# Kernel tuning notes

Measured on AMD Instinct MI355X. Metric: run time of the kernel, lower is better.

The kernel has to match this reference:

```python
import jax, jax.numpy as jnp
import numpy as np
from jax import lax

# norse LIFParameters defaults: dt=1e-3, tau_mem_inv=100, tau_syn_inv=200, v_leak=0, v_reset=0
ALPHA = 100.0
DT_TM = 0.1   # dt * tau_mem_inv
DT_TS = 0.2   # dt * tau_syn_inv

@jax.custom_vjp
def superspike(x):
    # Heaviside forward, SuperSpike surrogate gradient backward
    return (x > 0).astype(x.dtype)

def _ss_fwd(x):
    return superspike(x), x

def _ss_bwd(x, g):
    return (g / (ALPHA * jnp.abs(x) + 1.0) ** 2,)

superspike.defvjp(_ss_fwd, _ss_bwd)

def lif_step(inp, v, i, v_th):
    # norse lif_feed_forward_step (feedforward LIF cell)
    v_dec = v + DT_TM * (i - v)           # v_leak = 0
    i_dec = i * (1.0 - DT_TS)
    z = superspike(v_dec - v_th)
    v_new = (1.0 - z) * v_dec             # reset to v_reset = 0 on spike
    return z, v_new, i_dec + inp

def conv2d(x, w):
    return lax.conv_general_dilated(x, w, (1, 1), 'VALID',
                                    dimension_numbers=('NCHW', 'OIHW', 'NCHW'))

def avg_pool2(x):
    s = lax.reduce_window(x, jnp.zeros((), x.dtype), lax.add,
                          (1, 1, 2, 2), (1, 1, 2, 2), 'VALID')
    return s * jnp.asarray(0.25, x.dtype)

def setup_inputs() -> dict:
    key = jax.random.key(0)
    ks = jax.random.split(key, 6)
    x = jax.random.uniform(ks[0], (40, 256, 1, 28, 28), dtype=jnp.float32)
    # kaiming-ish scales (1/sqrt(fan_in))
    w_conv1 = jax.random.normal(ks[1], (20, 1, 3, 3), jnp.float32) * (1.0 / np.sqrt(9))
    w_conv2 = jax.random.normal(ks[2], (50, 20, 3, 3), jnp.float32) * (1.0 / np.sqrt(180))
    w_fc1 = jax.random.normal(ks[3], (500, 6050), jnp.float32) * (1.0 / np.sqrt(6050))
    w_fc2 = jax.random.normal(ks[4], (200, 500), jnp.float32) * (1.0 / np.sqrt(500))
    w_fc_out = jax.random.normal(ks[5], (10, 200), jnp.float32) * (1.0 / np.sqrt(200))
    return {"x": x, "w_conv1": w_conv1, "w_conv2": w_conv2,
            "w_fc1": w_fc1, "w_fc2": w_fc2, "w_fc_out": w_fc_out}

def reference(x, w_conv1, w_conv2, w_fc1, w_fc2, w_fc_out):
    T, B = x.shape[0], x.shape[1]
    dt = x.dtype
    z0 = jnp.zeros((B, 20, 26, 26), dt)
    z1 = jnp.zeros((B, 50, 11, 11), dt)
    z2 = jnp.zeros((B, 500), dt)
    z3 = jnp.zeros((B, 200), dt)
    zo = jnp.zeros((B, 10), dt)
    carry0 = (z0, z0, z1, z1, z2, z2, z3, z3, zo, zo)

    def step(carry, xt):
        v0, i0, v1, i1, v2, i2, v3, i3, vo, io = carry
        z = conv2d(xt, w_conv1)
        z, v0, i0 = lif_step(z, v0, i0, 0.2)
        z = avg_pool2(z)
        z = conv2d(z, w_conv2)
        z, v1, i1 = lif_step(z, v1, i1, 0.2)
        z = z.reshape(B, -1)                      # [B, 50*11*11]
        z = z @ w_fc1.T
        z, v2, i2 = lif_step(z, v2, i2, 0.1)
        z = z @ w_fc2.T
        z, v3, i3 = lif_step(z, v3, i3, 0.05)
        z = z @ w_fc_out.T
        # LICell (norse li_feed_forward_step): output is decayed membrane voltage
        v_dec = vo + DT_TM * (io - vo)
        i_new = io * (1.0 - DT_TS) + z
        return (v0, i0, v1, i1, v2, i2, v3, i3, v_dec, i_new), v_dec

    _, voltages = lax.scan(step, carry0, x)
    return voltages  # [T, B, output_neurons]
```

## Files before the change

kernel.cpp:

```cpp
#include <hip/hip_runtime.h>
#include <hip/hip_bf16.h>

typedef _Float16 f16x8 __attribute__((ext_vector_type(8)));
typedef float f32x4  __attribute__((ext_vector_type(4)));
typedef int   i32x4  __attribute__((ext_vector_type(4)));
typedef unsigned short u16x4 __attribute__((ext_vector_type(4)));

#define T_STEPS 40
#define BATCH   256
#define S2LO    0.000244140625f
#define WQ_INV  (2080768.0f/0.103f)
#define WQ_S    (0.103f/2080768.0f)

__device__ __forceinline__ unsigned short f2h_bits(float f) {
    union { _Float16 h; unsigned short u; } c; c.h = (_Float16)f; return c.u;
}

__device__ __forceinline__ float lif_update(float inp, float& v, float& i, float vth) {
    float vd = __fadd_rn(v, __fmul_rn(0.1f, __fsub_rn(i, v)));
    float id = __fmul_rn(0.8f, i);
    float z  = (vd > vth) ? 1.0f : 0.0f;
    v = (vd > vth) ? 0.0f : vd;
    i = __fadd_rn(id, inp);
    return z;
}

__device__ __forceinline__ void llds16(const void* g, void* l) {
    __builtin_amdgcn_global_load_lds(
        (const __attribute__((address_space(1))) unsigned int*)g,
        (__attribute__((address_space(3))) unsigned int*)l, 16, 0, 0);
}

__global__ __launch_bounds__(512) void k_conv1(
    const float* __restrict__ x,
    const float* __restrict__ w1,
    unsigned char* __restrict__ s0)
{
    const int b    = blockIdx.y;
    const int tid  = threadIdx.x;
    const int cell = blockIdx.x*512 + tid;
    const int pos  = cell / 24;
    const int oc   = cell - pos*24;
    const bool active = (pos < 169) && (oc < 20);
    const int pr   = pos / 13, q = pos - pr*13;
    const int r0   = 2*pr, c0 = 2*q;

    __shared__ __align__(16) float xl[4][784];
    const bool stager = tid < 196;

    float wr[9];
    if (active) {
        #pragma unroll
        for (int j = 0; j < 9; ++j) wr[j] = w1[oc*9 + j];
    }
    float vs[2][2], is[2][2];
    #pragma unroll
    for (int dr = 0; dr < 2; ++dr)
        #pragma unroll
        for (int dc = 0; dc < 2; ++dc) { vs[dr][dc] = 0.f; is[dr][dc] = 0.f; }

    float4 pA, pB;
    if (stager) {
        *(float4*)&xl[0][tid*4] = ((const float4*)(x + (size_t)(0*BATCH + b)*784))[tid];
        *(float4*)&xl[1][tid*4] = ((const float4*)(x + (size_t)(1*BATCH + b)*784))[tid];
        pA = ((const float4*)(x + (size_t)(2*BATCH + b)*784))[tid];
        pB = ((const float4*)(x + (size_t)(3*BATCH + b)*784))[tid];
    }

    for (int t = 0; t < T_STEPS; ++t) {
        __syncthreads();
        if (stager) {
            if (t + 2 < T_STEPS) *(float4*)&xl[(t+2)&3][tid*4] = pA;
            pA = pB;
            if (t + 4 < T_STEPS)
                pB = ((const float4*)(x + (size_t)((t+4)*BATCH + b)*784))[tid];
        }
        const float* xc = xl[t&3];
        size_t base = (size_t)(t*BATCH + b) * 4096;

        unsigned char outb = 0;
        if (active) {
            float tle[4][4];
            #pragma unroll
            for (int r = 0; r < 4; ++r) {
                float2 t01 = *(const float2*)&xc[(r0 + r)*28 + c0];
                float2 t23 = *(const float2*)&xc[(r0 + r)*28 + c0 + 2];
                tle[r][0] = t01.x; tle[r][1] = t01.y;
                tle[r][2] = t23.x; tle[r][3] = t23.y;
            }
            int zsum = 0;
            #pragma unroll
            for (int dr = 0; dr < 2; ++dr)
                #pragma unroll
                for (int dc = 0; dc < 2; ++dc) {
                    float acc = 0.f;
                    #pragma unroll
                    for (int kr = 0; kr < 3; ++kr)
                        #pragma unroll
                        for (int kc = 0; kc < 3; ++kc)
                            acc += tle[dr+kr][dc+kc] * wr[kr*3+kc];
                    float z = lif_update(acc, vs[dr][dc], is[dr][dc], 0.2f);
                    zsum += (z > 0.5f) ? 1 : 0;
                }
            outb = (unsigned char)zsum;
        }
        s0[base + cell] = outb;
    }
}

__global__ __launch_bounds__(256, 4) void k_conv2(
    const unsigned char* __restrict__ s0,
    const float* __restrict__ w2,
    unsigned char* __restrict__ z1)
{
    const int b    = blockIdx.x >> 2;
    const int quad = blockIdx.x & 3;
    const int tid  = threadIdx.x;
    const int wv   = tid >> 6;
    const int lane = tid & 63;
    const int l15  = lane & 15;
    const int kg   = lane >> 4;
    const int wm   = wv;

    __shared__ __align__(16) unsigned short w2h[16*232];
    __shared__ __align__(16) unsigned short w2m[16*232];
    __shared__ __align__(16) unsigned short sIn[2*4096];

    for (int s = tid; s < 16*232; s += 256) {
        int ocw = s / 232, kk = s % 232;
        int g = kk / 24, ic = kk % 24;
        int oc = quad*16 + ocw;
        float val = 0.f;
        if (oc < 50 && g < 9 && ic < 20) val = 0.25f * w2[(oc*20 + ic)*9 + g];
        _Float16 h = (_Float16)val;
        float r1 = (val - (float)h) * 4096.0f;
        union { _Float16 h; unsigned short u; } ch, cm;
        ch.h = h; cm.h = (_Float16)r1;
        w2h[s] = ch.u;
        w2m[s] = cm.u;
    }

    f16x8 bfrH[7];
    int addrA[2][7];
    #pragma unroll
    for (int mt = 0; mt < 2; ++mt) {
        int pos = wm*32 + mt*16 + l15;
        #pragma unroll
        for (int kt = 0; kt < 7; ++kt) {
            int k = kt*32 + kg*8;
            int g = k / 24, o = k - g*24;
            if (pos <= 120 && g <= 8) {
                int in_idx = pos + 2*(pos/11) + 13*(g/3) + (g % 3);
                addrA[mt][kt] = in_idx*48 + o*2;
            } else addrA[mt][kt] = 8128;
        }
    }

    {
        const unsigned char* srow = s0 + (size_t)(0*BATCH + b)*4096;
        uint4 raw = *(const uint4*)(srow + tid*16);
        unsigned short hv[16];
        #pragma unroll
        for (int w = 0; w < 4; ++w) {
            unsigned int u = ((const unsigned int*)&raw)[w];
            #pragma unroll
            for (int j = 0; j < 4; ++j)
                hv[w*4+j] = f2h_bits((float)((u >> (8*j)) & 0xFFu));
        }
        unsigned short* dst = sIn + tid*16;
        *(f16x8*)dst       = *(const f16x8*)&hv[0];
        *(f16x8*)(dst + 8) = *(const f16x8*)&hv[8];
    }
    __syncthreads();

    #pragma unroll
    for (int kt = 0; kt < 7; ++kt)
        bfrH[kt] = *(const f16x8*)&w2h[l15*232 + kt*32 + kg*8];

    float vst[2][4], ist[2][4];
    #pragma unroll
    for (int mt = 0; mt < 2; ++mt)
        #pragma unroll
        for (int r = 0; r < 4; ++r) { vst[mt][r] = 0.f; ist[mt][r] = 0.f; }

    const f32x4 zero4 = {0.f, 0.f, 0.f, 0.f};

    for (int t = 0; t < T_STEPS; ++t) {
        if (t > 0) __syncthreads();

        uint4 raw;
        if (t + 1 < T_STEPS)
            raw = *(const uint4*)(s0 + (size_t)((t+1)*BATCH + b)*4096 + tid*16);

        const char* curB = (const char*)(sIn + (t&1)*4096);

        f32x4 acch[2], accl[2];
        #pragma unroll
        for (int mt = 0; mt < 2; ++mt) { acch[mt] = zero4; accl[mt] = zero4; }

        #pragma unroll
        for (int kt = 0; kt < 7; ++kt) {
            f16x8 bm = *(const f16x8*)&w2m[l15*232 + kt*32 + kg*8];
            #pragma unroll
            for (int mt = 0; mt < 2; ++mt) {
                f16x8 a = *(const f16x8*)(curB + addrA[mt][kt]);
                acch[mt] = __builtin_amdgcn_mfma_f32_16x16x32_f16(
                    a, bfrH[kt], acch[mt], 0, 0, 0);
                accl[mt] = __builtin_amdgcn_mfma_f32_16x16x32_f16(
                    a, bm, accl[mt], 0, 0, 0);
            }
        }

        size_t rowoff = (size_t)(t*BATCH + b) * 6272;
        #pragma unroll
        for (int mt = 0; mt < 2; ++mt) {
            int posb = wm*32 + mt*16 + kg*4;
            int ocn = quad*16 + l15;
            unsigned char pk[4];
            #pragma unroll
            for (int r = 0; r < 4; ++r) {
                float inp = __fadd_rn(acch[mt][r], __fmul_rn(S2LO, accl[mt][r]));
                float z = lif_update(inp, vst[mt][r], ist[mt][r], 0.2f);
                int pos = posb + r;
                pk[r] = (pos <= 120 && z > 0.5f) ? (unsigned char)1 : (unsigned char)0;
            }
            if (ocn < 50 && posb < 121)
                *(uchar4*)(z1 + rowoff + ocn*124 + posb) = *(const uchar4*)&pk[0];
        }
        if (quad == 0 && tid < 72) z1[rowoff + 6200 + tid] = 0;

        if (t + 1 < T_STEPS) {
            unsigned short hv[16];
            #pragma unroll
            for (int w = 0; w < 4; ++w) {
                unsigned int u = ((const unsigned int*)&raw)[w];
                #pragma unroll
                for (int j = 0; j < 4; ++j)
                    hv[w*4+j] = f2h_bits((float)((u >> (8*j)) & 0xFFu));
            }
            unsigned short* dst = sIn + ((t+1)&1)*4096 + tid*16;
            *(f16x8*)dst       = *(const f16x8*)&hv[0];
            *(f16x8*)(dst + 8) = *(const f16x8*)&hv[8];
        }
    }
}

__global__ __launch_bounds__(256, 4) void k_gemm_fc1(
    const unsigned char* __restrict__ A,
    const signed char* __restrict__ Bq,
    float* __restrict__ P)
{
    __shared__ __align__(16) unsigned char As[64*128];
    __shared__ __align__(16) unsigned char Bs[3*64*128];

    const int tid  = threadIdx.x;
    const int lane = tid & 63;
    const int wv   = tid >> 6;
    const int wm   = wv & 1, wn = wv >> 1;
    const int l15  = lane & 15, kg = lane >> 4;
    const int mbase = blockIdx.x * 64;
    const int nbase = blockIdx.y * 64;
    const int kz    = blockIdx.z;
    const int kb0   = kz * 3200;
    const int kiters = 25 - kz;

    float* Pz = P + (size_t)kz * 5242880;

    i32x4 acc[3][2][2];
    #pragma unroll
    for (int p = 0; p < 3; ++p)
        #pragma unroll
        for (int mt = 0; mt < 2; ++mt)
            #pragma unroll
            for (int nt = 0; nt < 2; ++nt) acc[p][mt][nt] = (i32x4){0,0,0,0};

    const int rowS = tid >> 3;
    const int chk  = tid & 7;
    char* ldsA = (char*)As + (size_t)wv*1024;
    char* ldsB = (char*)Bs + (size_t)wv*1024;

    for (int ki = 0; ki < kiters; ++ki) {
        int kb = kb0 + ki * 128;
        #pragma unroll
        for (int c = 0; c < 2; ++c) {
            int rl = c*32 + rowS;
            llds16(A + (size_t)(mbase + rl)*6272 + kb + 16*(chk ^ (rl & 7)),
                   ldsA + c*4096);
        }
        #pragma unroll
        for (int p = 0; p < 3; ++p)
            #pragma unroll
            for (int c2 = 0; c2 < 2; ++c2) {
                int rl = c2*32 + rowS;
                llds16(Bq + (size_t)p*3211264 + (size_t)(nbase + rl)*6272
                          + kb + 16*(chk ^ (rl & 7)),
                       ldsB + (p*2 + c2)*4096);
            }
        __syncthreads();

        #pragma unroll
        for (int ks = 0; ks < 2; ++ks) {
            i32x4 afv[2], bfv[3][2];
            #pragma unroll
            for (int nt = 0; nt < 2; ++nt) {
                int rb = wn*32 + nt*16 + l15;
                int off = rb*128 + 16*((ks*4 + kg) ^ (rb & 7));
                #pragma unroll
                for (int p = 0; p < 3; ++p)
                    bfv[p][nt] = *(const i32x4*)&Bs[p*8192 + off];
            }
            #pragma unroll
            for (int mt = 0; mt < 2; ++mt) {
                int ra = wm*32 + mt*16 + l15;
                afv[mt] = *(const i32x4*)&As[ra*128 + 16*((ks*4 + kg) ^ (ra & 7))];
            }
            #pragma unroll
            for (int p = 0; p < 3; ++p)
                #pragma unroll
                for (int mt = 0; mt < 2; ++mt)
                    #pragma unroll
                    for (int nt = 0; nt < 2; ++nt)
                        acc[p][mt][nt] = __builtin_amdgcn_mfma_i32_16x16x64_i8(
                            afv[mt], bfv[p][nt], acc[p][mt][nt], 0, 0, 0);
        }
        __syncthreads();
    }

    #pragma unroll
    for (int mt = 0; mt < 2; ++mt) {
        int m0 = mbase + wm*32 + mt*16 + kg*4;
        #pragma unroll
        for (int nt = 0; nt < 2; ++nt) {
            int n = nbase + wn*32 + nt*16 + l15;
            #pragma unroll
            for (int r = 0; r < 4; ++r) {
                float d = __fadd_rn(
                    __fadd_rn(__fmul_rn(16384.0f, (float)acc[2][mt][nt][r]),
                              __fmul_rn(128.0f,   (float)acc[1][mt][nt][r])),
                    (float)acc[0][mt][nt][r]);
                Pz[(size_t)(m0 + r)*512 + n] = __fmul_rn(WQ_S, d);
            }
        }
    }
}

__global__ __launch_bounds__(256, 3) void k_gemm(
    const unsigned short* __restrict__ A,
    const unsigned short* __restrict__ B0,
    float* __restrict__ C0,
    int Kp, int kiters, int ldc, int nstore,
    size_t strideB, size_t strideC)
{
    __shared__ __align__(16) unsigned short As[128*64];
    __shared__ __align__(16) unsigned short Bs[128*64];
    const unsigned short* B = B0 + (size_t)blockIdx.z * strideB;
    float* C = C0 + (size_t)blockIdx.z * strideC;

    const int tid  = threadIdx.x;
    const int lane = tid & 63;
    const int wv   = tid >> 6;
    const int wm   = wv & 1, wn = wv >> 1;
    const int l15  = lane & 15, kg = lane >> 4;
    const int mbase = blockIdx.x * 128;
    const int nbase = blockIdx.y * 128;

    const f32x4 zero4 = {0.f, 0.f, 0.f, 0.f};
    f32x4 acc[4][4];
    #pragma unroll
    for (int mt = 0; mt < 4; ++mt)
        #pragma unroll
        for (int nt = 0; nt < 4; ++nt) acc[mt][nt] = zero4;

    const int rowA = tid >> 3;
    const int sw   = (((tid & 7) ^ (rowA & 7))) * 8;
    char* ldsA = (char*)As + (size_t)wv*1024;
    char* ldsB = (char*)Bs + (size_t)wv*1024;

    for (int ki = 0; ki < kiters; ++ki) {
        int kb = ki * 64;
        #pragma unroll
        for (int c = 0; c < 4; ++c) {
            int row = c*32 + rowA;
            llds16(A + (size_t)(mbase + row)*Kp + kb + sw, ldsA + c*4096);
            llds16(B + (size_t)(nbase + row)*Kp + kb + sw, ldsB + c*4096);
        }
        __syncthreads();
        #pragma unroll
        for (int kt = 0; kt < 2; ++kt) {
            f16x8 bfv[4], afv[4];
            #pragma unroll
            for (int nt = 0; nt < 4; ++nt) {
                int rb = wn*64 + nt*16 + l15;
                int ch = ((kt*4 + kg) ^ (rb & 7)) * 8;
                bfv[nt] = *(const f16x8*)&Bs[rb*64 + ch];
            }
            #pragma unroll
            for (int mt = 0; mt < 4; ++mt) {
                int ra = wm*64 + mt*16 + l15;
                int ch = ((kt*4 + kg) ^ (ra & 7)) * 8;
                afv[mt] = *(const f16x8*)&As[ra*64 + ch];
            }
            #pragma unroll
            for (int mt = 0; mt < 4; ++mt)
                #pragma unroll
                for (int nt = 0; nt < 4; ++nt)
                    acc[mt][nt] = __builtin_amdgcn_mfma_f32_16x16x32_f16(
                        afv[mt], bfv[nt], acc[mt][nt], 0, 0, 0);
        }
        __syncthreads();
    }

    #pragma unroll
    for (int mt = 0; mt < 4; ++mt) {
        int m0 = mbase + wm*64 + mt*16 + kg*4;
        #pragma unroll
        for (int nt = 0; nt < 4; ++nt) {
            int n = nbase + wn*64 + nt*16 + l15;
            if (n < nstore) {
                #pragma unroll
                for (int r = 0; r < 4; ++r)
                    C[(size_t)(m0 + r)*ldc + n] = acc[mt][nt][r];
            }
        }
    }
}

__global__ void k_pack_all(
    const float* __restrict__ wf1, const float* __restrict__ wf2,
    signed char* __restrict__ W1, unsigned short* __restrict__ W2)
{
    int idx = blockIdx.x*256 + threadIdx.x;
    if (idx < 3211264) {
        int n = idx / 6272, k = idx - n*6272;
        int oc = k / 124, pos = k - oc*124;
        float v = (n < 500 && oc < 50 && pos < 121) ? wf1[n*6050 + oc*121 + pos] : 0.f;
        float a = v * WQ_INV;
        int q2 = __float2int_rn(a * (1.0f/16384.0f));
        q2 = q2 < -127 ? -127 : (q2 > 127 ? 127 : q2);
        float r1 = a - (float)q2 * 16384.0f;
        int q1 = __float2int_rn(r1 * (1.0f/128.0f));
        q1 = q1 < -127 ? -127 : (q1 > 127 ? 127 : q1);
        float r0 = r1 - (float)q1 * 128.0f;
        int q0 = __float2int_rn(r0);
        q0 = q0 < -127 ? -127 : (q0 > 127 ? 127 : q0);
        W1[idx]             = (signed char)q0;
        W1[idx + 3211264]   = (signed char)q1;
        W1[idx + 2*3211264] = (signed char)q2;
        return;
    }
    if (idx < 3211264 + 131072) {
        int i2 = idx - 3211264;
        int n = i2 >> 9, k = i2 & 511;
        float v = (n < 200 && k < 500) ? wf2[n*500 + k] : 0.f;
        _Float16 h = (_Float16)v;
        float r1 = (v - (float)h) * 4096.0f;
        union { _Float16 h; unsigned short u; } ch, cl;
        ch.h = h; cl.h = (_Float16)r1;
        W2[i2] = ch.u;
        W2[i2 + 131072] = cl.u;
    }
}

__global__ void k_lif_scan(
    const float* __restrict__ c0, size_t pstride,
    unsigned short* __restrict__ zout,
    int ld, int nvalid, float vth, float pscale)
{
    int b = blockIdx.y;
    int n = blockIdx.x*blockDim.x + threadIdx.x;
    float v = 0.f, cur = 0.f;
    const float* sx = c0 + (size_t)b*ld + n;
    const float* sy = sx + pstride;
    const size_t step = (size_t)BATCH*ld;
    float x0 = sx[0],      y0 = sy[0];
    float x1 = sx[step],   y1 = sy[step];
    float x2 = sx[2*step], y2 = sy[2*step];
    float x3 = sx[3*step], y3 = sy[3*step];

    #define LIF_SUB(J, XV, YV)                                                \
        {                                                                     \
            float s = __fadd_rn(XV, __fmul_rn(pscale, YV));                   \
            float z = lif_update(s, v, cur, vth);                             \
            zout[(size_t)((t+J)*BATCH + b)*ld + n] =                          \
                (n < nvalid && z > 0.5f) ? (unsigned short)0x3C00             \
                                         : (unsigned short)0;                 \
            if (t + J + 4 < T_STEPS) {                                        \
                XV = sx[(size_t)(t + J + 4)*step];                            \
                YV = sy[(size_t)(t + J + 4)*step];                            \
            }                                                                 \
        }

    for (int t = 0; t < T_STEPS; t += 4) {
        LIF_SUB(0, x0, y0);
        LIF_SUB(1, x1, y1);
        LIF_SUB(2, x2, y2);
        LIF_SUB(3, x3, y3);
    }
    #undef LIF_SUB
}

__global__ __launch_bounds__(256) void k_sc2_fcout_li(
    const float* __restrict__ c3, size_t pstride,
    const float* __restrict__ wfo,
    float* __restrict__ out)
{
    const int b   = blockIdx.x;
    const int tid = threadIdx.x;
    __shared__ __align__(16) float wfoL[2000];
    __shared__ unsigned char z3L[T_STEPS*200];
    __shared__ float sL[400];

    for (int i = tid; i < 2000; i += 256) wfoL[i] = wfo[i];

    if (tid < 200) {
        const float* sx = c3 + (size_t)b*256 + tid;
        const float* sy = sx + pstride;
        const size_t step = (size_t)BATCH*256;
        float v = 0.f, cur = 0.f;
        float x0 = sx[0],      y0 = sy[0];
        float x1 = sx[step],   y1 = sy[step];
        float x2 = sx[2*step], y2 = sy[2*step];
        float x3 = sx[3*step], y3 = sy[3*step];

        #define SC2_SUB(J, XV, YV)                                            \
            {                                                                 \
                float s = __fadd_rn(XV, __fmul_rn(S2LO, YV));                 \
                float z = lif_update(s, v, cur, 0.05f);                       \
                z3L[(t+J)*200 + tid] = (z > 0.5f) ? 1 : 0;                    \
                if (t + J + 4 < T_STEPS) {                                    \
                    XV = sx[(size_t)(t + J + 4)*step];                        \
                    YV = sy[(size_t)(t + J + 4)*step];                        \
                }                                                             \
            }

        for (int t = 0; t < T_STEPS; t += 4) {
            SC2_SUB(0, x0, y0);
            SC2_SUB(1, x1, y1);
            SC2_SUB(2, x2, y2);
            SC2_SUB(3, x3, y3);
        }
        #undef SC2_SUB
    }
    __syncthreads();

    #pragma unroll
    for (int rep = 0; rep < 2; ++rep) {
        int task = tid + rep*256;
        if (task < 400) {
            int t = task / 10, n = task - t*10;
            float acc = 0.f;
            for (int k = 0; k < 200; k += 4) {
                uchar4 zb = *(const uchar4*)&z3L[t*200 + k];
                float4 wv = *(const float4*)&wfoL[n*200 + k];
                acc = __fadd_rn(acc, zb.x ? wv.x : 0.f);
                acc = __fadd_rn(acc, zb.y ? wv.y : 0.f);
                acc = __fadd_rn(acc, zb.z ? wv.z : 0.f);
                acc = __fadd_rn(acc, zb.w ? wv.w : 0.f);
            }
            sL[t*10 + n] = acc;
        }
    }
    __syncthreads();

    if (tid < 10) {
        float vo = 0.f, io = 0.f;
        for (int t = 0; t < T_STEPS; ++t) {
            float vd = __fadd_rn(vo, __fmul_rn(0.1f, __fsub_rn(io, vo)));
            out[((size_t)(t*BATCH + b))*10 + tid] = vd;
            io = __fadd_rn(__fmul_rn(0.8f, io), sL[t*10 + tid]);
            vo = vd;
        }
    }
}

extern "C" void kernel_launch(void* const* d_in, const int* in_sizes, int n_in,
                              void* d_out, int out_size, void* d_ws, size_t ws_size,
                              hipStream_t stream) {
    (void)in_sizes; (void)n_in; (void)out_size; (void)ws_size;
    const float* x   = (const float*)d_in[0];
    const float* w1  = (const float*)d_in[1];
    const float* w2  = (const float*)d_in[2];
    const float* wf1 = (const float*)d_in[3];
    const float* wf2 = (const float*)d_in[4];
    const float* wfo = (const float*)d_in[5];
    char* ws = (char*)d_ws;

    unsigned char*  z1    = (unsigned char*)(ws);
    unsigned char*  s0    = (unsigned char*)(ws + 64225280);
    signed char*    W1q   = (signed char*)(ws + 64225280);
    unsigned short* W2hi  = (unsigned short*)(ws + 73859072);
    float*          c2p   = (float*)(ws + 74383360);
    unsigned short* z2    = (unsigned short*)(ws);
    float*          c3p   = (float*)(ws + 10485760);

    k_conv1<<<dim3(8, 256), 512, 0, stream>>>(x, w1, s0);
    k_conv2<<<1024, 256, 0, stream>>>(s0, w2, z1);

    k_pack_all<<<13056, 256, 0, stream>>>(wf1, wf2, W1q, W2hi);

    k_gemm_fc1<<<dim3(160, 8, 2), 256, 0, stream>>>(z1, W1q, c2p);
    k_lif_scan<<<dim3(2, 256), 256, 0, stream>>>(c2p, (size_t)5242880, z2, 512, 500, 0.1f, 1.0f);
    k_gemm<<<dim3(80,2,2), 256, 0, stream>>>(z2, W2hi, c3p, 512, 8, 256, 256,
                                             (size_t)131072, (size_t)2621440);
    k_sc2_fcout_li<<<256, 256, 0, stream>>>(c3p, (size_t)2621440, wfo, (float*)d_out);
}
```

Measured before the change: 371.5 us.

## Fuse weight packing into conv1 and combine fc2 hi/lo split GEMM

Weight quantization/packing now runs on extra blocks appended to the conv1 grid, which removes a separate launch and lets it overlap with conv1. The packed weights move to their own workspace region so they no longer alias s0. The fc2 GEMM becomes a dedicated 64x64-tile kernel that accumulates the hi and lo fp16 weight halves in one pass and writes a combined result. This removes the second partial buffer and the extra add in the final scan. The fc1 GEMM is split into two launches over halves of M, which adds a launch but may help scheduling.

```diff
diff --git a/kernel.cpp b/kernel.cpp
--- a/kernel.cpp
+++ b/kernel.cpp
@@ -34,8 +34,47 @@
 __global__ __launch_bounds__(512) void k_conv1(
     const float* __restrict__ x,
     const float* __restrict__ w1,
-    unsigned char* __restrict__ s0)
+    unsigned char* __restrict__ s0,
+    const float* __restrict__ wf1,
+    const float* __restrict__ wf2,
+    signed char* __restrict__ W1,
+    unsigned short* __restrict__ W2)
 {
+    if (blockIdx.y >= 256) {
+        int pid = (blockIdx.y - 256)*8 + blockIdx.x;
+        for (int idx = pid*512 + threadIdx.x; idx < 3342336; idx += 106496) {
+            if (idx < 3211264) {
+                int n = idx / 6272, k = idx - n*6272;
+                int oc = k / 124, pos = k - oc*124;
+                float v = (n < 500 && oc < 50 && pos < 121)
+                          ? wf1[n*6050 + oc*121 + pos] : 0.f;
+                float a = v * WQ_INV;
+                int q2 = __float2int_rn(a * (1.0f/16384.0f));
+                q2 = q2 < -127 ? -127 : (q2 > 127 ? 127 : q2);
+                float r1 = a - (float)q2 * 16384.0f;
+                int q1 = __float2int_rn(r1 * (1.0f/128.0f));
+                q1 = q1 < -127 ? -127 : (q1 > 127 ? 127 : q1);
+                float r0 = r1 - (float)q1 * 128.0f;
+                int q0 = __float2int_rn(r0);
+                q0 = q0 < -127 ? -127 : (q0 > 127 ? 127 : q0);
+                W1[idx]             = (signed char)q0;
+                W1[idx + 3211264]   = (signed char)q1;
+                W1[idx + 2*3211264] = (signed char)q2;
+            } else {
+                int i2 = idx - 3211264;
+                int n = i2 >> 9, k = i2 & 511;
+                float v = (n < 200 && k < 500) ? wf2[n*500 + k] : 0.f;
+                _Float16 h = (_Float16)v;
+                float r1 = (v - (float)h) * 4096.0f;
+                union { _Float16 h; unsigned short u; } ch, cl;
+                ch.h = h; cl.h = (_Float16)r1;
+                W2[i2] = ch.u;
+                W2[i2 + 131072] = cl.u;
+            }
+        }
+        return;
+    }
+
     const int b    = blockIdx.y;
     const int tid  = threadIdx.x;
     const int cell = blockIdx.x*512 + tid;
@@ -248,10 +287,111 @@
 __global__ __launch_bounds__(256, 4) void k_gemm_fc1(
     const unsigned char* __restrict__ A,
     const signed char* __restrict__ Bq,
-    float* __restrict__ P)
+    float* __restrict__ P,
+    int mb0)
 {
     __shared__ __align__(16) unsigned char As[64*128];
     __shared__ __align__(16) unsigned char Bs[3*64*128];
+
+    const int tid  = threadIdx.x;
+    const int lane = tid & 63;
+    const int wv   = tid >> 6;
+    const int wm   = wv & 1, wn = wv >> 1;
+    const int l15  = lane & 15, kg = lane >> 4;
+    const int mbase = (blockIdx.x + mb0) * 64;
+    const int nbase = blockIdx.y * 64;
+    const int kz    = blockIdx.z;
+    const int kb0   = kz * 3200;
+    const int kiters = 25 - kz;
+
+    float* Pz = P + (size_t)kz * 5242880;
+
+    i32x4 acc[3][2][2];
+    #pragma unroll
+    for (int p = 0; p < 3; ++p)
+        #pragma unroll
+        for (int mt = 0; mt < 2; ++mt)
+            #pragma unroll
+            for (int nt = 0; nt < 2; ++nt) acc[p][mt][nt] = (i32x4){0,0,0,0};
+
+    const int rowS = tid >> 3;
+    const int chk  = tid & 7;
+    char* ldsA = (char*)As + (size_t)wv*1024;
+    char* ldsB = (char*)Bs + (size_t)wv*1024;
+
+    for (int ki = 0; ki < kiters; ++ki) {
+        int kb = kb0 + ki * 128;
+        #pragma unroll
+        for (int c = 0; c < 2; ++c) {
+            int rl = c*32 + rowS;
+            llds16(A + (size_t)(mbase + rl)*6272 + kb + 16*(chk ^ (rl & 7)),
+                   ldsA + c*4096);
+        }
+        #pragma unroll
+        for (int p = 0; p < 3; ++p)
+            #pragma unroll
+            for (int c2 = 0; c2 < 2; ++c2) {
+                int rl = c2*32 + rowS;
+                llds16(Bq + (size_t)p*3211264 + (size_t)(nbase + rl)*6272
+                          + kb + 16*(chk ^ (rl & 7)),
+                       ldsB + (p*2 + c2)*4096);
+            }
+        __syncthreads();
+
+        #pragma unroll
+        for (int ks = 0; ks < 2; ++ks) {
+            i32x4 afv[2], bfv[3][2];
+            #pragma unroll
+            for (int nt = 0; nt < 2; ++nt) {
+                int rb = wn*32 + nt*16 + l15;
+                int off = rb*128 + 16*((ks*4 + kg) ^ (rb & 7));
+                #pragma unroll
+                for (int p = 0; p < 3; ++p)
+                    bfv[p][nt] = *(const i32x4*)&Bs[p*8192 + off];
+            }
+            #pragma unroll
+            for (int mt = 0; mt < 2; ++mt) {
+                int ra = wm*32 + mt*16 + l15;
+                afv[mt] = *(const i32x4*)&As[ra*128 + 16*((ks*4 + kg) ^ (ra & 7))];
+            }
+            #pragma unroll
+            for (int p = 0; p < 3; ++p)
+                #pragma unroll
+                for (int mt = 0; mt < 2; ++mt)
+                    #pragma unroll
+                    for (int nt = 0; nt < 2; ++nt)
+                        acc[p][mt][nt] = __builtin_amdgcn_mfma_i32_16x16x64_i8(
+                            afv[mt], bfv[p][nt], acc[p][mt][nt], 0, 0, 0);
+        }
+        __syncthreads();
+    }
+
+    #pragma unroll
+    for (int mt = 0; mt < 2; ++mt) {
+        int m0 = mbase + wm*32 + mt*16 + kg*4;
+        #pragma unroll
+        for (int nt = 0; nt < 2; ++nt) {
+            int n = nbase + wn*32 + nt*16 + l15;
+            #pragma unroll
+            for (int r = 0; r < 4; ++r) {
+                float d = __fadd_rn(
+                    __fadd_rn(__fmul_rn(16384.0f, (float)acc[2][mt][nt][r]),
+                              __fmul_rn(128.0f,   (float)acc[1][mt][nt][r])),
+                    (float)acc[0][mt][nt][r]);
+                Pz[(size_t)(m0 + r)*512 + n] = __fmul_rn(WQ_S, d);
+            }
+        }
+    }
+}
+
+__global__ __launch_bounds__(256, 6) void k_gemm_fc2(
+    const unsigned short* __restrict__ A,
+    const unsigned short* __restrict__ B,
+    float* __restrict__ C)
+{
+    __shared__ __align__(16) unsigned short As[64*64];
+    __shared__ __align__(16) unsigned short Bh[64*64];
+    __shared__ __align__(16) unsigned short Bl[64*64];
 
     const int tid  = threadIdx.x;
     const int lane = tid & 63;
@@ -260,68 +400,57 @@
     const int l15  = lane & 15, kg = lane >> 4;
     const int mbase = blockIdx.x * 64;
     const int nbase = blockIdx.y * 64;
-    const int kz    = blockIdx.z;
-    const int kb0   = kz * 3200;
-    const int kiters = 25 - kz;
-
-    float* Pz = P + (size_t)kz * 5242880;
-
-    i32x4 acc[3][2][2];
-    #pragma unroll
-    for (int p = 0; p < 3; ++p)
-        #pragma unroll
-        for (int mt = 0; mt < 2; ++mt)
-            #pragma unroll
-            for (int nt = 0; nt < 2; ++nt) acc[p][mt][nt] = (i32x4){0,0,0,0};
+    const unsigned short* Blo = B + 131072;
+
+    const f32x4 zero4 = {0.f, 0.f, 0.f, 0.f};
+    f32x4 acch[2][2], accl[2][2];
+    #pragma unroll
+    for (int mt = 0; mt < 2; ++mt)
+        #pragma unroll
+        for (int nt = 0; nt < 2; ++nt) { acch[mt][nt] = zero4; accl[mt][nt] = zero4; }
 
     const int rowS = tid >> 3;
     const int chk  = tid & 7;
     char* ldsA = (char*)As + (size_t)wv*1024;
-    char* ldsB = (char*)Bs + (size_t)wv*1024;
-
-    for (int ki = 0; ki < kiters; ++ki) {
-        int kb = kb0 + ki * 128;
+    char* ldsH = (char*)Bh + (size_t)wv*1024;
+    char* ldsL = (char*)Bl + (size_t)wv*1024;
+
+    for (int ki = 0; ki < 8; ++ki) {
+        int kb = ki * 64;
         #pragma unroll
         for (int c = 0; c < 2; ++c) {
             int rl = c*32 + rowS;
-            llds16(A + (size_t)(mbase + rl)*6272 + kb + 16*(chk ^ (rl & 7)),
-                   ldsA + c*4096);
-        }
-        #pragma unroll
-        for (int p = 0; p < 3; ++p)
-            #pragma unroll
-            for (int c2 = 0; c2 < 2; ++c2) {
-                int rl = c2*32 + rowS;
-                llds16(Bq + (size_t)p*3211264 + (size_t)(nbase + rl)*6272
-                          + kb + 16*(chk ^ (rl & 7)),
-                       ldsB + (p*2 + c2)*4096);
-            }
+            int sw = (chk ^ (rl & 7)) * 8;
+            llds16(A   + (size_t)(mbase + rl)*512 + kb + sw, ldsA + c*4096);
+            llds16(B   + (size_t)(nbase + rl)*512 + kb + sw, ldsH + c*4096);
+            llds16(Blo + (size_t)(nbase + rl)*512 + kb + sw, ldsL + c*4096);
+        }
         __syncthreads();
-
-        #pragma unroll
-        for (int ks = 0; ks < 2; ++ks) {
-            i32x4 afv[2], bfv[3][2];
+        #pragma unroll
+        for (int kt = 0; kt < 2; ++kt) {
+            f16x8 bh[2], bl[2], afv[2];
             #pragma unroll
             for (int nt = 0; nt < 2; ++nt) {
                 int rb = wn*32 + nt*16 + l15;
-                int off = rb*128 + 16*((ks*4 + kg) ^ (rb & 7));
-                #pragma unroll
-                for (int p = 0; p < 3; ++p)
-                    bfv[p][nt] = *(const i32x4*)&Bs[p*8192 + off];
+                int ch = ((kt*4 + kg) ^ (rb & 7)) * 8;
+                bh[nt] = *(const f16x8*)&Bh[rb*64 + ch];
+                bl[nt] = *(const f16x8*)&Bl[rb*64 + ch];
             }
             #pragma unroll
             for (int mt = 0; mt < 2; ++mt) {
                 int ra = wm*32 + mt*16 + l15;
-                afv[mt] = *(const i32x4*)&As[ra*128 + 16*((ks*4 + kg) ^ (ra & 7))];
-            }
-            #pragma unroll
-            for (int p = 0; p < 3; ++p)
+                int ch = ((kt*4 + kg) ^ (ra & 7)) * 8;
+                afv[mt] = *(const f16x8*)&As[ra*64 + ch];
+            }
+            #pragma unroll
+            for (int mt = 0; mt < 2; ++mt)
                 #pragma unroll
-                for (int mt = 0; mt < 2; ++mt)
-                    #pragma unroll
-                    for (int nt = 0; nt < 2; ++nt)
-                        acc[p][mt][nt] = __builtin_amdgcn_mfma_i32_16x16x64_i8(
-                            afv[mt], bfv[p][nt], acc[p][mt][nt], 0, 0, 0);
+                for (int nt = 0; nt < 2; ++nt) {
+                    acch[mt][nt] = __builtin_amdgcn_mfma_f32_16x16x32_f16(
+                        afv[mt], bh[nt], acch[mt][nt], 0, 0, 0);
+                    accl[mt][nt] = __builtin_amdgcn_mfma_f32_16x16x32_f16(
+                        afv[mt], bl[nt], accl[mt][nt], 0, 0, 0);
+                }
         }
         __syncthreads();
     }
@@ -334,130 +463,10 @@
             int n = nbase + wn*32 + nt*16 + l15;
             #pragma unroll
             for (int r = 0; r < 4; ++r) {
-                float d = __fadd_rn(
-                    __fadd_rn(__fmul_rn(16384.0f, (float)acc[2][mt][nt][r]),
-                              __fmul_rn(128.0f,   (float)acc[1][mt][nt][r])),
-                    (float)acc[0][mt][nt][r]);
-                Pz[(size_t)(m0 + r)*512 + n] = __fmul_rn(WQ_S, d);
-            }
-        }
-    }
-}
-
-__global__ __launch_bounds__(256, 3) void k_gemm(
-    const unsigned short* __restrict__ A,
-    const unsigned short* __restrict__ B0,
-    float* __restrict__ C0,
-    int Kp, int kiters, int ldc, int nstore,
-    size_t strideB, size_t strideC)
-{
-    __shared__ __align__(16) unsigned short As[128*64];
-    __shared__ __align__(16) unsigned short Bs[128*64];
-    const unsigned short* B = B0 + (size_t)blockIdx.z * strideB;
-    float* C = C0 + (size_t)blockIdx.z * strideC;
-
-    const int tid  = threadIdx.x;
-    const int lane = tid & 63;
-    const int wv   = tid >> 6;
-    const int wm   = wv & 1, wn = wv >> 1;
-    const int l15  = lane & 15, kg = lane >> 4;
-    const int mbase = blockIdx.x * 128;
-    const int nbase = blockIdx.y * 128;
-
-    const f32x4 zero4 = {0.f, 0.f, 0.f, 0.f};
-    f32x4 acc[4][4];
-    #pragma unroll
-    for (int mt = 0; mt < 4; ++mt)
-        #pragma unroll
-        for (int nt = 0; nt < 4; ++nt) acc[mt][nt] = zero4;
-
-    const int rowA = tid >> 3;
-    const int sw   = (((tid & 7) ^ (rowA & 7))) * 8;
-    char* ldsA = (char*)As + (size_t)wv*1024;
-    char* ldsB = (char*)Bs + (size_t)wv*1024;
-
-    for (int ki = 0; ki < kiters; ++ki) {
-        int kb = ki * 64;
-        #pragma unroll
-        for (int c = 0; c < 4; ++c) {
-            int row = c*32 + rowA;
-            llds16(A + (size_t)(mbase + row)*Kp + kb + sw, ldsA + c*4096);
-            llds16(B + (size_t)(nbase + row)*Kp + kb + sw, ldsB + c*4096);
-        }
-        __syncthreads();
-        #pragma unroll
-        for (int kt = 0; kt < 2; ++kt) {
-            f16x8 bfv[4], afv[4];
-            #pragma unroll
-            for (int nt = 0; nt < 4; ++nt) {
-                int rb = wn*64 + nt*16 + l15;
-                int ch = ((kt*4 + kg) ^ (rb & 7)) * 8;
-                bfv[nt] = *(const f16x8*)&Bs[rb*64 + ch];
-            }
-            #pragma unroll
-            for (int mt = 0; mt < 4; ++mt) {
-                int ra = wm*64 + mt*16 + l15;
-                int ch = ((kt*4 + kg) ^ (ra & 7)) * 8;
-                afv[mt] = *(const f16x8*)&As[ra*64 + ch];
-            }
-            #pragma unroll
-            for (int mt = 0; mt < 4; ++mt)
-                #pragma unroll
-                for (int nt = 0; nt < 4; ++nt)
-                    acc[mt][nt] = __builtin_amdgcn_mfma_f32_16x16x32_f16(
-                        afv[mt], bfv[nt], acc[mt][nt], 0, 0, 0);
-        }
-        __syncthreads();
-    }
-
-    #pragma unroll
-    for (int mt = 0; mt < 4; ++mt) {
-        int m0 = mbase + wm*64 + mt*16 + kg*4;
-        #pragma unroll
-        for (int nt = 0; nt < 4; ++nt) {
-            int n = nbase + wn*64 + nt*16 + l15;
-            if (n < nstore) {
-                #pragma unroll
-                for (int r = 0; r < 4; ++r)
-                    C[(size_t)(m0 + r)*ldc + n] = acc[mt][nt][r];
-            }
-        }
-    }
-}
-
-__global__ void k_pack_all(
-    const float* __restrict__ wf1, const float* __restrict__ wf2,
-    signed char* __restrict__ W1, unsigned short* __restrict__ W2)
-{
-    int idx = blockIdx.x*256 + threadIdx.x;
-    if (idx < 3211264) {
-        int n = idx / 6272, k = idx - n*6272;
-        int oc = k / 124, pos = k - oc*124;
-        float v = (n < 500 && oc < 50 && pos < 121) ? wf1[n*6050 + oc*121 + pos] : 0.f;
-        float a = v * WQ_INV;
-        int q2 = __float2int_rn(a * (1.0f/16384.0f));
-        q2 = q2 < -127 ? -127 : (q2 > 127 ? 127 : q2);
-        float r1 = a - (float)q2 * 16384.0f;
-        int q1 = __float2int_rn(r1 * (1.0f/128.0f));
-        q1 = q1 < -127 ? -127 : (q1 > 127 ? 127 : q1);
-        float r0 = r1 - (float)q1 * 128.0f;
-        int q0 = __float2int_rn(r0);
-        q0 = q0 < -127 ? -127 : (q0 > 127 ? 127 : q0);
-        W1[idx]             = (signed char)q0;
-        W1[idx + 3211264]   = (signed char)q1;
-        W1[idx + 2*3211264] = (signed char)q2;
-        return;
-    }
-    if (idx < 3211264 + 131072) {
-        int i2 = idx - 3211264;
-        int n = i2 >> 9, k = i2 & 511;
-        float v = (n < 200 && k < 500) ? wf2[n*500 + k] : 0.f;
-        _Float16 h = (_Float16)v;
-        float r1 = (v - (float)h) * 4096.0f;
-        union { _Float16 h; unsigned short u; } ch, cl;
-        ch.h = h; cl.h = (_Float16)r1;
-        W2[i2] = ch.u;
-        W2[i2 + 131072] = cl.u;
+                float s = __fadd_rn(acch[mt][nt][r], __fmul_rn(S2LO, accl[mt][nt][r]));
+                C[(size_t)(m0 + r)*256 + n] = s;
+            }
+        }
     }
 }
 
@@ -500,7 +509,7 @@
 }
 
 __global__ __launch_bounds__(256) void k_sc2_fcout_li(
-    const float* __restrict__ c3, size_t pstride,
+    const float* __restrict__ c3,
     const float* __restrict__ wfo,
     float* __restrict__ out)
 {
@@ -514,30 +523,23 @@
 
     if (tid < 200) {
         const float* sx = c3 + (size_t)b*256 + tid;
-        const float* sy = sx + pstride;
         const size_t step = (size_t)BATCH*256;
         float v = 0.f, cur = 0.f;
-        float x0 = sx[0],      y0 = sy[0];
-        float x1 = sx[step],   y1 = sy[step];
-        float x2 = sx[2*step], y2 = sy[2*step];
-        float x3 = sx[3*step], y3 = sy[3*step];
-
-        #define SC2_SUB(J, XV, YV)                                            \
+        float x0 = sx[0], x1 = sx[step], x2 = sx[2*step], x3 = sx[3*step];
+
+        #define SC2_SUB(J, XV)                                                \
             {                                                                 \
-                float s = __fadd_rn(XV, __fmul_rn(S2LO, YV));                 \
-                float z = lif_update(s, v, cur, 0.05f);                       \
+                float z = lif_update(XV, v, cur, 0.05f);                      \
                 z3L[(t+J)*200 + tid] = (z > 0.5f) ? 1 : 0;                    \
-                if (t + J + 4 < T_STEPS) {                                    \
+                if (t + J + 4 < T_STEPS)                                      \
                     XV = sx[(size_t)(t + J + 4)*step];                        \
-                    YV = sy[(size_t)(t + J + 4)*step];                        \
-                }                                                             \
             }
 
         for (int t = 0; t < T_STEPS; t += 4) {
-            SC2_SUB(0, x0, y0);
-            SC2_SUB(1, x1, y1);
-            SC2_SUB(2, x2, y2);
-            SC2_SUB(3, x3, y3);
+            SC2_SUB(0, x0);
+            SC2_SUB(1, x1);
+            SC2_SUB(2, x2);
+            SC2_SUB(3, x3);
         }
         #undef SC2_SUB
     }
@@ -587,20 +589,18 @@
 
     unsigned char*  z1    = (unsigned char*)(ws);
     unsigned char*  s0    = (unsigned char*)(ws + 64225280);
-    signed char*    W1q   = (signed char*)(ws + 64225280);
-    unsigned short* W2hi  = (unsigned short*)(ws + 73859072);
     float*          c2p   = (float*)(ws + 74383360);
+    signed char*    W1q   = (signed char*)(ws + 116326400);
+    unsigned short* W2hi  = (unsigned short*)(ws + 125960192);
     unsigned short* z2    = (unsigned short*)(ws);
-    float*          c3p   = (float*)(ws + 10485760);
-
-    k_conv1<<<dim3(8, 256), 512, 0, stream>>>(x, w1, s0);
+    float*          c3    = (float*)(ws + 10485760);
+
+    k_conv1<<<dim3(8, 282), 512, 0, stream>>>(x, w1, s0, wf1, wf2, W1q, W2hi);
     k_conv2<<<1024, 256, 0, stream>>>(s0, w2, z1);
 
-    k_pack_all<<<13056, 256, 0, stream>>>(wf1, wf2, W1q, W2hi);
-
-    k_gemm_fc1<<<dim3(160, 8, 2), 256, 0, stream>>>(z1, W1q, c2p);
+    k_gemm_fc1<<<dim3(80, 8, 2), 256, 0, stream>>>(z1, W1q, c2p, 0);
+    k_gemm_fc1<<<dim3(80, 8, 2), 256, 0, stream>>>(z1, W1q, c2p, 80);
     k_lif_scan<<<dim3(2, 256), 256, 0, stream>>>(c2p, (size_t)5242880, z2, 512, 500, 0.1f, 1.0f);
-    k_gemm<<<dim3(80,2,2), 256, 0, stream>>>(z2, W2hi, c3p, 512, 8, 256, 256,
-                                             (size_t)131072, (size_t)2621440);
-    k_sc2_fcout_li<<<256, 256, 0, stream>>>(c3p, (size_t)2621440, wfo, (float*)d_out);
-}
+    k_gemm_fc2<<<dim3(160, 4), 256, 0, stream>>>(z2, W2hi, c3);
+    k_sc2_fcout_li<<<256, 256, 0, stream>>>(c3, wfo, (float*)d_out);
+}
```

After: 390.9 us. +5.2%, slower.
